# Kernel optimization log

Hardware: AMD Instinct MI355X
Metric: run time of the kernel (lower is better)

## Reference

```python
import jax, jax.numpy as jnp
import numpy as np

KERNEL_SIZE = (3, 3)
STRIDE = 1
PADDING = 'valid'  # 'valid' -> no padding; 'same' -> pad per module's pad_tensor


def setup_inputs() -> dict:
    key = jax.random.key(0)
    kx, kk = jax.random.split(key)
    C_in, H, W = 16, 2048, 2048
    C_out = 16
    hf, wf = KERNEL_SIZE
    x = jax.random.normal(kx, (C_in, H, W), dtype=jnp.float32)
    kernels = jax.random.normal(kk, (C_out, C_in, hf, wf), dtype=jnp.float32)
    return {"x": x, "kernels": kernels}


def _conv(x, kernels):
    # x: (C,H,W); kernels: (C_out,C_in,hf,wf)
    # The torch module's im2col + mm is exactly a cross-correlation (no kernel
    # flip), i.e., standard conv in DL convention.
    if PADDING == 'same':
        hf, wf = KERNEL_SIZE
        ph, pw = (hf - 1) // 2, (wf - 1) // 2
        # NOTE: original ConstantPad3d((0,0,pad_h,pad_h,pad_w,pad_w)) pads H by
        # pad_h and C by pad_w on a (C,H,W) tensor; for square kernels with
        # hf==wf the intended symmetric spatial pad is equivalent here.
        x = jnp.pad(x, ((0, 0), (ph, ph), (pw, pw)))
    out = jax.lax.conv_general_dilated(
        x[None],                      # (1,C,H,W)
        kernels,                      # (O,I,hf,wf)
        window_strides=(STRIDE, STRIDE),
        padding='VALID',
        dimension_numbers=('NCHW', 'OIHW', 'NCHW'),
    )
    return out[0]                     # (C_out,H_out,W_out)


def reference(x, kernels):
    return _conv(x, kernels)
```

## Files before the change

kernel.cpp:

```cpp
#include <hip/hip_runtime.h>


#define HIN   2048
#define WIN   2048
#define HOUT  2046
#define WOUT  2046
#define PLANE_IN  (HIN * WIN)
#define PLANE_OUT (HOUT * WOUT)
#define TR 34
#define TC 36
#define NQTASK (TR * 9 * 2)
#define WF_U32 (5 * 64 * 4)

typedef __attribute__((ext_vector_type(8))) short bf16x8;
typedef __attribute__((ext_vector_type(4))) float f32x4;
typedef __attribute__((ext_vector_type(4))) unsigned u32x4;
typedef f32x4 __attribute__((aligned(4))) f32x4_u;

static __device__ __forceinline__ short f2bf(float f) {
    unsigned u = __float_as_uint(f);
    return (short)((u + 0x7FFFu + ((u >> 16) & 1u)) >> 16);
}
static __device__ __forceinline__ unsigned pk2(float lo, float hi) {
    unsigned a = __float_as_uint(lo);
    unsigned b = __float_as_uint(hi);
    a = (a + 0x7FFFu + ((a >> 16) & 1u)) >> 16;
    b = (b + 0x7FFFu + ((b >> 16) & 1u)) & 0xFFFF0000u;
    return a | b;
}

__global__ __launch_bounds__(64)
void wf_setup(const float* __restrict__ k, unsigned* __restrict__ wfbuf) {
    int lane = threadIdx.x;
    int m = lane & 15, g = lane >> 4;
    #pragma unroll
    for (int i = 0; i < 5; ++i) {
        u32x4 q;
        #pragma unroll
        for (int jj = 0; jj < 4; ++jj) {
            unsigned r = 0;
            #pragma unroll
            for (int e = 0; e < 2; ++e) {
                int kk  = 32 * i + 8 * g + 2 * jj + e;
                int tap = kk >> 4;
                int ci  = kk & 15;
                unsigned v = 0;
                if (tap < 9) v = (unsigned short)f2bf(k[(m * 16 + ci) * 9 + tap]);
                r |= v << (16 * e);
            }
            q[jj] = r;
        }
        *(u32x4*)(wfbuf + (i * 64 + lane) * 4) = q;
    }
}

#define GLOADX4(DST, ADDR) \
    asm volatile("global_load_dwordx4 %0, %1, off" : "=&v"(DST) : "v"(ADDR))

__global__ __launch_bounds__(1024, 2)
void conv3x3_fused1k(const float* __restrict__ x,
                     const unsigned* __restrict__ wfbuf,
                     float* __restrict__ out) {
    __shared__ unsigned lds[TR * TC * 8];

    const int tid  = threadIdx.x;
    const int lane = tid & 63;
    const int wv   = tid >> 6;
    const int m    = lane & 15;
    const int g    = lane >> 4;

    int bid = blockIdx.x;
    int swz = (bid & 7) * 512 + (bid >> 3);
    int h0 = (swz >> 6) * 32; if (h0 > HOUT - 32) h0 = HOUT - 32;
    int w0 = (swz & 63) * 32;

    if (tid < NQTASK) {
        int t   = tid;
        int q   = t % 9;
        int r2  = t / 9;
        int cih = r2 & 1;
        int row = r2 >> 1;
        int c   = 4 * q;
        int w   = w0 + c; if (w > WIN - 4) w = WIN - 4;
        const float* gp = x + (size_t)(cih * 8) * PLANE_IN
                            + (size_t)(h0 + row) * WIN + w;
        f32x4 f0, f1, f2, f3, f4, f5, f6, f7;
        GLOADX4(f0, gp + 0 * (size_t)PLANE_IN);
        GLOADX4(f1, gp + 1 * (size_t)PLANE_IN);
        GLOADX4(f2, gp + 2 * (size_t)PLANE_IN);
        GLOADX4(f3, gp + 3 * (size_t)PLANE_IN);
        GLOADX4(f4, gp + 4 * (size_t)PLANE_IN);
        GLOADX4(f5, gp + 5 * (size_t)PLANE_IN);
        GLOADX4(f6, gp + 6 * (size_t)PLANE_IN);
        GLOADX4(f7, gp + 7 * (size_t)PLANE_IN);
        asm volatile("s_waitcnt vmcnt(0)" ::: "memory");
        __builtin_amdgcn_sched_barrier(0);

        int a = ((row * TC + c) * 32 + cih * 16) ^ ((c & 4) << 2);
        u32x4 ch;
        ch[0] = pk2(f0[0], f1[0]); ch[1] = pk2(f2[0], f3[0]);
        ch[2] = pk2(f4[0], f5[0]); ch[3] = pk2(f6[0], f7[0]);
        *(u32x4*)((char*)lds + a)      = ch;
        ch[0] = pk2(f0[1], f1[1]); ch[1] = pk2(f2[1], f3[1]);
        ch[2] = pk2(f4[1], f5[1]); ch[3] = pk2(f6[1], f7[1]);
        *(u32x4*)((char*)lds + a + 32) = ch;
        ch[0] = pk2(f0[2], f1[2]); ch[1] = pk2(f2[2], f3[2]);
        ch[2] = pk2(f4[2], f5[2]); ch[3] = pk2(f6[2], f7[2]);
        *(u32x4*)((char*)lds + a + 64) = ch;
        ch[0] = pk2(f0[3], f1[3]); ch[1] = pk2(f2[3], f3[3]);
        ch[2] = pk2(f4[3], f5[3]); ch[3] = pk2(f6[3], f7[3]);
        *(u32x4*)((char*)lds + a + 96) = ch;
    }

    bf16x8 wf[5];
    #pragma unroll
    for (int i = 0; i < 5; ++i)
        wf[i] = *(const bf16x8*)(wfbuf + (i * 64 + lane) * 4);

    int off[5];
    #pragma unroll
    for (int i = 0; i < 5; ++i) {
        int tap = 2 * i + (g >> 1);
        if (tap > 8) tap = 8;
        int kh = tap / 3;
        int kw = tap - kh * 3;
        int col = m + kw;
        int o = (kh * TC + col) * 32 + (g & 1) * 16;
        off[i] = o ^ ((col & 4) << 2);
    }

    __syncthreads();

    const char* ldsb = (const char*)lds;

    #pragma unroll
    for (int hl2 = 0; hl2 < 2; ++hl2) {
        int hl = wv * 2 + hl2;
        int h  = h0 + hl;
        #pragma unroll
        for (int nh = 0; nh < 2; ++nh) {
            int wl = nh * 16;
            int tb = (hl * TC + wl) * 32;
            f32x4 acc = {0.f, 0.f, 0.f, 0.f};
            #pragma unroll
            for (int i = 0; i < 5; ++i) {
                bf16x8 a = *(const bf16x8*)(ldsb + (tb + off[i]));
                acc = __builtin_amdgcn_mfma_f32_16x16x32_bf16(a, wf[i], acc, 0, 0, 0);
            }
            int w = w0 + wl + g * 4;
            float* op = out + m * (size_t)PLANE_OUT + (size_t)h * WOUT + w;
            if (w + 3 < WOUT) {
                *(f32x4_u*)op = acc;
            } else {
                #pragma unroll
                for (int r = 0; r < 4; ++r)
                    if (w + r < WOUT) op[r] = acc[r];
            }
        }
    }
}

__global__ __launch_bounds__(256, 4)
void conv3x3_mfma(const float* __restrict__ x,
                  const float* __restrict__ k,
                  float* __restrict__ out) {
    __shared__ short lds2[TR * 34 * 16];
    const int tid  = threadIdx.x;
    const int lane = tid & 63;
    const int wv   = tid >> 6;
    const int m    = lane & 15;
    const int g    = lane >> 4;
    int bid = blockIdx.x;
    int swz = (bid & 7) * 512 + (bid >> 3);
    int h0 = (swz >> 6) * 32;
    int w0 = (swz & 63) * 32;
    for (int p = tid; p < TR * 34; p += 256) {
        int r = p / 34, c = p - r * 34;
        int hh = h0 + r; if (hh > HIN - 1) hh = HIN - 1;
        int ww = w0 + c; if (ww > WIN - 1) ww = WIN - 1;
        const float* gp = x + hh * WIN + ww;
        short t[16];
        #pragma unroll
        for (int ci = 0; ci < 16; ++ci) t[ci] = f2bf(gp[ci * PLANE_IN]);
        bf16x8 lo, hi;
        #pragma unroll
        for (int j = 0; j < 8; ++j) { lo[j] = t[j]; hi[j] = t[8 + j]; }
        int sw = (c >> 2) & 1;
        bf16x8* dst = (bf16x8*)&lds2[p * 16];
        dst[sw] = lo; dst[1 - sw] = hi;
    }
    bf16x8 wf[5];
    #pragma unroll
    for (int i = 0; i < 5; ++i)
        #pragma unroll
        for (int j = 0; j < 8; ++j) {
            int kk = 32 * i + 8 * g + j;
            int tap = kk >> 4, ci = kk & 15;
            short v = 0;
            if (tap < 9) v = f2bf(k[(m * 16 + ci) * 9 + tap]);
            wf[i][j] = v;
        }
    int off[5];
    #pragma unroll
    for (int i = 0; i < 5; ++i) {
        int tap = 2 * i + (g >> 1);
        if (tap > 8) tap = 8;
        int kh = tap / 3, kw = tap - kh * 3;
        int col = m + kw;
        int o = (kh * 34 + col) * 32 + (g & 1) * 16;
        off[i] = o ^ ((col & 4) << 2);
    }
    __syncthreads();
    const char* ldsb = (const char*)lds2;
    const int coBase = g * 4;
    for (int hl8 = 0; hl8 < 8; ++hl8) {
        int hl = wv * 8 + hl8;
        int h = h0 + hl;
        bool hok = (h < HOUT);
        #pragma unroll
        for (int nh = 0; nh < 2; ++nh) {
            int wl = nh * 16;
            int tb = (hl * 34 + wl) * 32;
            f32x4 acc = {0.f, 0.f, 0.f, 0.f};
            #pragma unroll
            for (int i = 0; i < 5; ++i) {
                bf16x8 b = *(const bf16x8*)(ldsb + (tb + off[i]));
                acc = __builtin_amdgcn_mfma_f32_16x16x32_bf16(wf[i], b, acc, 0, 0, 0);
            }
            int w = w0 + wl + m;
            if (hok && w < WOUT) {
                float* op = out + h * WOUT + w;
                #pragma unroll
                for (int r = 0; r < 4; ++r)
                    op[(coBase + r) * PLANE_OUT] = acc[r];
            }
        }
    }
}

extern "C" void kernel_launch(void* const* d_in, const int* in_sizes, int n_in,
                              void* d_out, int out_size, void* d_ws, size_t ws_size,
                              hipStream_t stream) {
    const float* x = (const float*)d_in[0];
    const float* k = (const float*)d_in[1];
    float* out = (float*)d_out;
    if (ws_size >= WF_U32 * 4) {
        unsigned* wfbuf = (unsigned*)d_ws;
        wf_setup<<<dim3(1), dim3(64), 0, stream>>>(k, wfbuf);
        conv3x3_fused1k<<<dim3(4096), dim3(1024), 0, stream>>>(x, wfbuf, out);
    } else {
        conv3x3_mfma<<<dim3(4096), dim3(256), 0, stream>>>(x, k, out);
    }
}
```

Measured before the change: 152.6 us.

## Add persistent double-buffered conv kernel overlapping global loads with MFMA compute

Adds a new kernel in which each 1024-thread block walks eight 32-wide tiles along a 256-column strip. While MFMA computes on the current LDS buffer, the global loads for the next tile are already in flight into a second LDS buffer. The grid drops from 4096 to 512 blocks, and the kernel requests about 78 KB of dynamic shared memory per block. The aim is to hide load latency and cut block launch overhead, at the cost of occupancy and tail balance with fewer blocks. It also changes the fallback kernel's inline-asm loads to plain vector loads.

Result: slower. 218.0 us (+42.9%).

```diff
diff --git a/kernel.cpp b/kernel.cpp
--- a/kernel.cpp
+++ b/kernel.cpp
@@ -10,6 +10,7 @@
 #define TR 34
 #define TC 36
 #define NQTASK (TR * 9 * 2)
+#define BUFB (TR * TC * 32)
 #define WF_U32 (5 * 64 * 4)
 
 typedef __attribute__((ext_vector_type(8))) short bf16x8;
@@ -58,6 +59,144 @@
     asm volatile("global_load_dwordx4 %0, %1, off" : "=&v"(DST) : "v"(ADDR))
 
 __global__ __launch_bounds__(1024, 2)
+void conv3x3_pipe(const float* __restrict__ x,
+                  const unsigned* __restrict__ wfbuf,
+                  float* __restrict__ out) {
+    extern __shared__ unsigned lds[];
+
+    const int tid  = threadIdx.x;
+    const int lane = tid & 63;
+    const int wv   = tid >> 6;
+    const int m    = lane & 15;
+    const int g    = lane >> 4;
+
+    int bid   = blockIdx.x;
+    int swz   = (bid & 7) * 64 + (bid >> 3);
+    int htile = swz >> 3;
+    int strip = swz & 7;
+    int h0 = htile * 32; if (h0 > HOUT - 32) h0 = HOUT - 32;
+    const int wbase = strip * 256;
+
+    const bool has = (tid < NQTASK);
+    int q = 0, cih = 0, row = 0, c = 0, abase = 0;
+    const float* gpr = x;
+    if (has) {
+        q   = tid % 9;
+        int r2 = tid / 9;
+        cih = r2 & 1;
+        row = r2 >> 1;
+        c   = 4 * q;
+        gpr = x + (size_t)(cih * 8) * PLANE_IN + (size_t)(h0 + row) * WIN;
+        abase = ((row * TC + c) * 32 + cih * 16) ^ ((c & 4) << 2);
+    }
+
+    int off[5];
+    #pragma unroll
+    for (int i = 0; i < 5; ++i) {
+        int tap = 2 * i + (g >> 1);
+        if (tap > 8) tap = 8;
+        int kh = tap / 3;
+        int kw = tap - kh * 3;
+        int col = m + kw;
+        int o = (kh * TC + col) * 32 + (g & 1) * 16;
+        off[i] = o ^ ((col & 4) << 2);
+    }
+
+    f32x4 f0, f1, f2, f3, f4, f5, f6, f7;
+
+#define ISSUE(W0) do {                                                        \
+        if (has) {                                                            \
+            int w = (W0) + c; if (w > WIN - 4) w = WIN - 4;                   \
+            const float* gp = gpr + w;                                        \
+            GLOADX4(f0, gp + 0 * (size_t)PLANE_IN);                           \
+            GLOADX4(f1, gp + 1 * (size_t)PLANE_IN);                           \
+            GLOADX4(f2, gp + 2 * (size_t)PLANE_IN);                           \
+            GLOADX4(f3, gp + 3 * (size_t)PLANE_IN);                           \
+            GLOADX4(f4, gp + 4 * (size_t)PLANE_IN);                           \
+            GLOADX4(f5, gp + 5 * (size_t)PLANE_IN);                           \
+            GLOADX4(f6, gp + 6 * (size_t)PLANE_IN);                           \
+            GLOADX4(f7, gp + 7 * (size_t)PLANE_IN);                           \
+        }                                                                     \
+        __builtin_amdgcn_sched_barrier(0);                                    \
+    } while (0)
+
+#define PACK(BUFOFF) do {                                                     \
+        if (has) {                                                            \
+            char* dst = (char*)lds + (BUFOFF) + abase;                        \
+            u32x4 ch;                                                         \
+            ch[0] = pk2(f0[0], f1[0]); ch[1] = pk2(f2[0], f3[0]);             \
+            ch[2] = pk2(f4[0], f5[0]); ch[3] = pk2(f6[0], f7[0]);             \
+            *(u32x4*)(dst)      = ch;                                         \
+            ch[0] = pk2(f0[1], f1[1]); ch[1] = pk2(f2[1], f3[1]);             \
+            ch[2] = pk2(f4[1], f5[1]); ch[3] = pk2(f6[1], f7[1]);             \
+            *(u32x4*)(dst + 32) = ch;                                         \
+            ch[0] = pk2(f0[2], f1[2]); ch[1] = pk2(f2[2], f3[2]);             \
+            ch[2] = pk2(f4[2], f5[2]); ch[3] = pk2(f6[2], f7[2]);             \
+            *(u32x4*)(dst + 64) = ch;                                         \
+            ch[0] = pk2(f0[3], f1[3]); ch[1] = pk2(f2[3], f3[3]);             \
+            ch[2] = pk2(f4[3], f5[3]); ch[3] = pk2(f6[3], f7[3]);             \
+            *(u32x4*)(dst + 96) = ch;                                         \
+        }                                                                     \
+    } while (0)
+
+#define COMPUTE(BUFOFF, W0) do {                                              \
+        const char* ldsb = (const char*)lds + (BUFOFF);                       \
+        bf16x8 wf[5];                                                         \
+        _Pragma("unroll")                                                     \
+        for (int i = 0; i < 5; ++i)                                           \
+            wf[i] = *(const bf16x8*)(wfbuf + (i * 64 + lane) * 4);            \
+        _Pragma("unroll")                                                     \
+        for (int hl2 = 0; hl2 < 2; ++hl2) {                                   \
+            int hl = wv * 2 + hl2;                                            \
+            int h  = h0 + hl;                                                 \
+            _Pragma("unroll")                                                 \
+            for (int nh = 0; nh < 2; ++nh) {                                  \
+                int wl = nh * 16;                                             \
+                int tb = (hl * TC + wl) * 32;                                 \
+                f32x4 acc = {0.f, 0.f, 0.f, 0.f};                             \
+                _Pragma("unroll")                                             \
+                for (int i = 0; i < 5; ++i) {                                 \
+                    bf16x8 a = *(const bf16x8*)(ldsb + (tb + off[i]));        \
+                    acc = __builtin_amdgcn_mfma_f32_16x16x32_bf16(            \
+                              a, wf[i], acc, 0, 0, 0);                        \
+                }                                                             \
+                int w = (W0) + wl + g * 4;                                    \
+                float* op = out + m * (size_t)PLANE_OUT                       \
+                                + (size_t)h * WOUT + w;                       \
+                if (w + 3 < WOUT) {                                           \
+                    *(f32x4_u*)op = acc;                                      \
+                } else {                                                      \
+                    _Pragma("unroll")                                         \
+                    for (int r = 0; r < 4; ++r)                               \
+                        if (w + r < WOUT) op[r] = acc[r];                     \
+                }                                                             \
+            }                                                                 \
+        }                                                                     \
+    } while (0)
+
+    ISSUE(wbase);
+    asm volatile("s_waitcnt vmcnt(0)" ::: "memory");
+    __builtin_amdgcn_sched_barrier(0);
+    PACK(0);
+    __syncthreads();
+
+    #pragma unroll 2
+    for (int t = 0; t < 8; ++t) {
+        const int buf  = (t & 1) * BUFB;
+        const int nbuf = ((t + 1) & 1) * BUFB;
+        if (t < 7) ISSUE(wbase + (t + 1) * 32);
+        COMPUTE(buf, wbase + t * 32);
+        asm volatile("s_waitcnt vmcnt(0)" ::: "memory");
+        __builtin_amdgcn_sched_barrier(0);
+        if (t < 7) PACK(nbuf);
+        __syncthreads();
+    }
+#undef ISSUE
+#undef PACK
+#undef COMPUTE
+}
+
+__global__ __launch_bounds__(1024, 2)
 void conv3x3_fused1k(const float* __restrict__ x,
                      const unsigned* __restrict__ wfbuf,
                      float* __restrict__ out) {
@@ -84,18 +223,14 @@
         int w   = w0 + c; if (w > WIN - 4) w = WIN - 4;
         const float* gp = x + (size_t)(cih * 8) * PLANE_IN
                             + (size_t)(h0 + row) * WIN + w;
-        f32x4 f0, f1, f2, f3, f4, f5, f6, f7;
-        GLOADX4(f0, gp + 0 * (size_t)PLANE_IN);
-        GLOADX4(f1, gp + 1 * (size_t)PLANE_IN);
-        GLOADX4(f2, gp + 2 * (size_t)PLANE_IN);
-        GLOADX4(f3, gp + 3 * (size_t)PLANE_IN);
-        GLOADX4(f4, gp + 4 * (size_t)PLANE_IN);
-        GLOADX4(f5, gp + 5 * (size_t)PLANE_IN);
-        GLOADX4(f6, gp + 6 * (size_t)PLANE_IN);
-        GLOADX4(f7, gp + 7 * (size_t)PLANE_IN);
-        asm volatile("s_waitcnt vmcnt(0)" ::: "memory");
-        __builtin_amdgcn_sched_barrier(0);
-
+        f32x4 f0 = *(const f32x4*)(gp + 0 * (size_t)PLANE_IN);
+        f32x4 f1 = *(const f32x4*)(gp + 1 * (size_t)PLANE_IN);
+        f32x4 f2 = *(const f32x4*)(gp + 2 * (size_t)PLANE_IN);
+        f32x4 f3 = *(const f32x4*)(gp + 3 * (size_t)PLANE_IN);
+        f32x4 f4 = *(const f32x4*)(gp + 4 * (size_t)PLANE_IN);
+        f32x4 f5 = *(const f32x4*)(gp + 5 * (size_t)PLANE_IN);
+        f32x4 f6 = *(const f32x4*)(gp + 6 * (size_t)PLANE_IN);
+        f32x4 f7 = *(const f32x4*)(gp + 7 * (size_t)PLANE_IN);
         int a = ((row * TC + c) * 32 + cih * 16) ^ ((c & 4) << 2);
         u32x4 ch;
         ch[0] = pk2(f0[0], f1[0]); ch[1] = pk2(f2[0], f3[0]);
@@ -247,7 +382,14 @@
     if (ws_size >= WF_U32 * 4) {
         unsigned* wfbuf = (unsigned*)d_ws;
         wf_setup<<<dim3(1), dim3(64), 0, stream>>>(k, wfbuf);
-        conv3x3_fused1k<<<dim3(4096), dim3(1024), 0, stream>>>(x, wfbuf, out);
+        hipError_t e = hipFuncSetAttribute(
+            reinterpret_cast<const void*>(conv3x3_pipe),
+            hipFuncAttributeMaxDynamicSharedMemorySize, 2 * BUFB);
+        if (e == hipSuccess) {
+            conv3x3_pipe<<<dim3(512), dim3(1024), 2 * BUFB, stream>>>(x, wfbuf, out);
+        } else {
+            conv3x3_fused1k<<<dim3(4096), dim3(1024), 0, stream>>>(x, wfbuf, out);
+        }
     } else {
         conv3x3_mfma<<<dim3(4096), dim3(256), 0, stream>>>(x, k, out);
     }
```
